# Performance work log

Hardware: AMD Instinct MI355X
Metric: run time of the kernel (lower is better)

## Reference

```python
import jax, jax.numpy as jnp
import numpy as np

N1 = 512
N2 = 512
N = N1 + N2
NEG_SLOPE = 0.2


def _build_edges(n1, n2):
    # inside: fully connected within each set, both directions
    s1, d1 = np.triu_indices(n1, 1)
    s2, d2 = np.triu_indices(n2, 1)
    is_ = np.concatenate([s1, s2 + n1])
    id_ = np.concatenate([d1, d2 + n1])
    inside = np.stack([np.concatenate([is_, id_]), np.concatenate([id_, is_])])
    # cross: fully connected bipartite, both directions
    cs = np.repeat(np.arange(n1), n2)
    cd = np.tile(np.arange(n1, n1 + n2), n1)
    cross = np.stack([np.concatenate([cs, cd]), np.concatenate([cd, cs])])
    # PyG GATConv default add_self_loops=True
    loops = np.arange(n1 + n2)
    self_e = np.stack([loops, loops])
    inside = np.concatenate([inside, self_e], axis=1)
    cross = np.concatenate([cross, self_e], axis=1)
    return inside.astype(np.int32), cross.astype(np.int32)


def setup_inputs() -> dict:
    key = jax.random.key(0)
    ks = jax.random.split(key, 12)
    inside_edge, cross_edge = _build_edges(N1, N2)
    s = 0.1
    return {
        'desc1': jax.random.normal(ks[0], (N1, 128), jnp.float32),
        'desc2': jax.random.normal(ks[1], (N2, 128), jnp.float32),
        'W1': jax.random.normal(ks[2], (128, 128), jnp.float32) * s,
        'a_src1': jax.random.normal(ks[3], (128, 1), jnp.float32) * s,
        'a_dst1': jax.random.normal(ks[4], (128, 1), jnp.float32) * s,
        'b1': jnp.zeros((128,), jnp.float32),
        'W2': jax.random.normal(ks[5], (128, 128), jnp.float32) * s,
        'a_src2': jax.random.normal(ks[6], (1, 128), jnp.float32) * s,
        'a_dst2': jax.random.normal(ks[7], (1, 128), jnp.float32) * s,
        'b2': jnp.zeros((128,), jnp.float32),
        'inside_edge': jnp.asarray(inside_edge),
        'cross_edge': jnp.asarray(cross_edge),
    }


def gat_conv(x, edge_index, W, a_src, a_dst, bias, heads, out_ch, concat):
    # x: [N, F_in]; edge_index: [2, E] (self-loops already included)
    n = x.shape[0]
    src, dst = edge_index[0], edge_index[1]
    h = (x @ W).reshape(n, heads, out_ch)                 # [N, H, C]
    a_s = jnp.sum(h * a_src, axis=-1)                     # [N, H]
    a_d = jnp.sum(h * a_dst, axis=-1)                     # [N, H]
    e = jax.nn.leaky_relu(a_s[src] + a_d[dst], NEG_SLOPE)  # [E, H]
    # segment (scatter) softmax over incoming edges of each dst node
    m = jax.ops.segment_max(e, dst, num_segments=n)
    ex = jnp.exp(e - m[dst])
    denom = jax.ops.segment_sum(ex, dst, num_segments=n)
    alpha = ex / (denom[dst] + 1e-16)                     # [E, H]
    out = jax.ops.segment_sum(alpha[:, :, None] * h[src], dst, num_segments=n)  # [N, H, C]
    out = out.reshape(n, heads * out_ch) if concat else out.mean(axis=1)
    return out + bias


def reference(desc1, desc2, W1, a_src1, a_dst1, b1, W2, a_src2, a_dst2, b2, inside_edge, cross_edge):
    x = jnp.concatenate([desc1, desc2], axis=0)  # [N, 128]
    for _ in range(2):
        x = jax.nn.elu(gat_conv(x, inside_edge, W1, a_src1, a_dst1, b1, 128, 1, True))
        x = jax.nn.elu(gat_conv(x, cross_edge, W1, a_src1, a_dst1, b1, 128, 1, True))
    x = gat_conv(x, cross_edge, W2, a_src2, a_dst2, b2, 1, 128, False)  # [N, 128]
    return x
```

## Files before the change

### kernel.cpp

```cpp
#include <hip/hip_runtime.h>
#include <hip/hip_bf16.h>


typedef __hip_bfloat16 bf16;

__device__ __forceinline__ float b2f(bf16 x) { return __bfloat162float(x); }

__device__ __forceinline__ int detect_bf16(const void* desc1) {
  const unsigned* u = (const unsigned*)desc1;
  int hits = 0;
#pragma unroll 8
  for (int i = 0; i < 256; ++i) {
    unsigned e = (u[i] >> 7) & 0xFFu;
    hits += (e >= 100u && e <= 140u) ? 1 : 0;
  }
  return hits >= 200 ? 1 : 0;
}

__device__ __forceinline__ float load_in(const void* p, int i, int bf) {
  return bf ? b2f(((const bf16*)p)[i]) : ((const float*)p)[i];
}

__global__ __launch_bounds__(256) void prep_kernel(
    const void* __restrict__ desc1, const void* __restrict__ desc2,
    const void* __restrict__ W1,   const void* __restrict__ as1,
    const void* __restrict__ ad1,  const void* __restrict__ b1,
    const void* __restrict__ W2,   const void* __restrict__ as2,
    const void* __restrict__ ad2,  const void* __restrict__ b2,
    float* __restrict__ xt, float* __restrict__ W1f, float* __restrict__ W2f,
    float* __restrict__ vecs, int* __restrict__ flag) {
  const int bf = detect_bf16(desc1);
  if (blockIdx.x == 0 && threadIdx.x == 0) *flag = bf;
  const int total = 131072 + 16384 + 16384 + 6 * 128;
  for (int idx = blockIdx.x * blockDim.x + threadIdx.x; idx < total;
       idx += gridDim.x * blockDim.x) {
    if (idx < 131072) {
      int n = idx & 1023, c = idx >> 10;
      float v = (n < 512) ? load_in(desc1, n * 128 + c, bf)
                          : load_in(desc2, (n - 512) * 128 + c, bf);
      xt[idx] = v;
    } else if (idx < 147456) {
      W1f[idx - 131072] = load_in(W1, idx - 131072, bf);
    } else if (idx < 163840) {
      W2f[idx - 147456] = load_in(W2, idx - 147456, bf);
    } else {
      int i = idx - 163840, o = i & 127;
      float v;
      if      (i < 128) v = load_in(as1, o, bf);
      else if (i < 256) v = load_in(ad1, o, bf);
      else if (i < 384) v = load_in(b1, o, bf);
      else if (i < 512) v = load_in(as2, o, bf);
      else if (i < 640) v = load_in(ad2, o, bf);
      else              v = load_in(b2, o, bf);
      vecs[i] = v;
    }
  }
}

template <int CROSS>
__global__ __launch_bounds__(512, 2) void layer_kernel(
    const float* __restrict__ xt_in, float* __restrict__ xt_out,
    const float* __restrict__ Wf, const float* __restrict__ vecs) {
  __shared__ float    sS[512];
  __shared__ float    sH[512];
  __shared__ unsigned hA[512];
  __shared__ unsigned ISb[512];
  __shared__ unsigned binNext[512];
  __shared__ float2   PRE[512];
  __shared__ float2   SUF[512];
  __shared__ float    red[16];
  __shared__ unsigned wTot[8];
  __shared__ float2   preTot[8];
  __shared__ float2   sufTot[8];

  const int tid  = threadIdx.x;
  const int lane = tid & 63;
  const int wave = tid >> 6;
  const int hd   = blockIdx.x & 127;
  const int S    = blockIdx.x >> 7;
  const int D    = CROSS ? (1 - S) : S;
  const float a_src = vecs[hd], a_dst = vecs[128 + hd], bias = vecs[256 + hd];

  float accS0 = 0.f, accS1 = 0.f, accD0 = 0.f, accD1 = 0.f;
  {
    const float* baseS = xt_in + S * 512 + tid;
    const float* baseD = xt_in + D * 512 + tid;
    for (int kk = 0; kk < 128; kk += 16) {
      float xs[16], xd[16];
#pragma unroll
      for (int u = 0; u < 16; ++u) {
        xs[u] = baseS[(kk + u) * 1024];
        if (CROSS) xd[u] = baseD[(kk + u) * 1024];
      }
#pragma unroll
      for (int u = 0; u < 16; u += 2) {
        float w0 = Wf[(kk + u) * 128 + hd];
        float w1 = Wf[(kk + u + 1) * 128 + hd];
        accS0 = fmaf(xs[u],     w0, accS0);
        accS1 = fmaf(xs[u + 1], w1, accS1);
        if (CROSS) {
          accD0 = fmaf(xd[u],     w0, accD0);
          accD1 = fmaf(xd[u + 1], w1, accD1);
        }
      }
    }
  }
  const float h_src = accS0 + accS1;
  const float h_dst = CROSS ? (accD0 + accD1) : h_src;
  const float s_own = h_src * a_src;
  const float d_own = h_dst * a_dst;

  {
    float mnw = s_own, mxw = s_own;
#pragma unroll
    for (int off = 32; off > 0; off >>= 1) {
      mnw = fminf(mnw, __shfl_down(mnw, off));
      mxw = fmaxf(mxw, __shfl_down(mxw, off));
    }
    if (lane == 0) { red[wave] = mnw; red[8 + wave] = mxw; }
  }
  hA[tid] = 0;
  binNext[tid] = 0;
  __syncthreads();
  const float mn = fminf(fminf(fminf(red[0], red[1]), fminf(red[2], red[3])),
                         fminf(fminf(red[4], red[5]), fminf(red[6], red[7])));
  const float mx = fmaxf(fmaxf(fmaxf(red[8], red[9]), fmaxf(red[10], red[11])),
                         fmaxf(fmaxf(red[12], red[13]), fmaxf(red[14], red[15])));
  const float scale = 512.0f / fmaxf(mx - mn, 1e-20f);

  const int myBin = (int)fminf(fmaxf((s_own - mn) * scale, 0.0f), 511.0f);
  atomicAdd(&hA[myBin], 1u);
  __syncthreads();

  {
    unsigned v = hA[tid];
#pragma unroll
    for (int off = 1; off < 64; off <<= 1) {
      unsigned u = __shfl_up(v, off);
      if (lane >= off) v += u;
    }
    if (lane == 63) wTot[wave] = v;
    __syncthreads();
    unsigned pre = 0;
#pragma unroll
    for (int w = 0; w < 8; ++w) pre += (w < wave) ? wTot[w] : 0u;
    ISb[tid] = v + pre;
    __syncthreads();
  }

  {
    unsigned base = myBin ? ISb[myBin - 1] : 0u;
    unsigned pos = base + atomicAdd(&binNext[myBin], 1u);
    sS[pos] = s_own;
    sH[pos] = h_src;
  }
  __syncthreads();

  {
    const float sv = sS[tid];
    const float hv = sH[tid];
    const float e1 = __expf(sv), e2 = __expf(0.2f * sv);
    float p0 = e2, p1 = e2 * hv;
    float q0 = e1, q1 = e1 * hv;
#pragma unroll
    for (int off = 1; off < 64; off <<= 1) {
      float u0 = __shfl_up(p0, off), u1 = __shfl_up(p1, off);
      if (lane >= off) { p0 += u0; p1 += u1; }
      float v0 = __shfl_down(q0, off), v1 = __shfl_down(q1, off);
      if (lane + off < 64) { q0 += v0; q1 += v1; }
    }
    if (lane == 63) preTot[wave] = make_float2(p0, p1);
    if (lane == 0)  sufTot[wave] = make_float2(q0, q1);
    __syncthreads();
    float a0 = 0.f, a1 = 0.f, b0 = 0.f, b1 = 0.f;
#pragma unroll
    for (int w = 0; w < 8; ++w) {
      float2 pt = preTot[w], st = sufTot[w];
      if (w < wave) { a0 += pt.x; a1 += pt.y; }
      if (w > wave) { b0 += st.x; b1 += st.y; }
    }
    PRE[tid] = make_float2(p0 + a0, p1 + a1);
    SUF[tid] = make_float2(q0 + b0, q1 + b1);
    __syncthreads();
  }

  {
    const float theta = -d_own;
    int b = (int)fminf(fmaxf((theta - mn) * scale, 0.0f), 511.0f);
    unsigned k0 = b ? ISb[b - 1] : 0u;
    unsigned k1 = ISb[b];
    float F1 = __expf(d_own), F2 = __expf(0.2f * d_own);
    float P2 = 0.f, P2h = 0.f, S1 = 0.f, S1h = 0.f;
    if (k0 > 0)   { float2 t2 = PRE[k0 - 1]; P2 = t2.x; P2h = t2.y; }
    if (k1 < 512) { float2 t2 = SUF[k1];     S1 = t2.x; S1h = t2.y; }
    float den = F1 * S1 + F2 * P2;
    float num = F1 * S1h + F2 * P2h;
    for (unsigned e = k0; e < k1; ++e) {
      float se = sS[e], he = sH[e];
      float p = (se >= theta) ? F1 * __expf(se) : F2 * __expf(0.2f * se);
      den += p;
      num = fmaf(p, he, num);
    }
    if (CROSS) {
      float t = h_dst * a_src + d_own;
      float p = __expf(fmaxf(t, 0.2f * t));
      den += p;
      num = fmaf(p, h_dst, num);
    }
    float o = num / (den + 1e-16f) + bias;
    o = (o > 0.f) ? o : expm1f(o);
    xt_out[hd * 1024 + D * 512 + tid] = o;
  }
}

__global__ __launch_bounds__(256, 2) void mm2_kernel(
    const float* __restrict__ xt_in, const float* __restrict__ W2f,
    const float* __restrict__ vecs, float* __restrict__ h2,
    float* __restrict__ s2, float* __restrict__ d2) {
  __shared__ float rs[256], rd[256];
  const int tid = threadIdx.x;
  const int row = blockIdx.x * 2 + (tid >> 7);
  const int c = tid & 127;
  float acc0 = 0.f, acc1 = 0.f;
  for (int kk = 0; kk < 128; kk += 16) {
    float xb[16];
#pragma unroll
    for (int u = 0; u < 16; ++u) xb[u] = xt_in[(kk + u) * 1024 + row];
#pragma unroll
    for (int u = 0; u < 16; u += 2) {
      acc0 = fmaf(xb[u],     W2f[(kk + u) * 128 + c],     acc0);
      acc1 = fmaf(xb[u + 1], W2f[(kk + u + 1) * 128 + c], acc1);
    }
  }
  float acc = acc0 + acc1;
  h2[row * 128 + c] = acc;
  rs[tid] = acc * vecs[384 + c];
  rd[tid] = acc * vecs[512 + c];
  __syncthreads();
  for (int off = 64; off > 0; off >>= 1) {
    if ((tid & 127) < off) { rs[tid] += rs[tid + off]; rd[tid] += rd[tid + off]; }
    __syncthreads();
  }
  if ((tid & 127) == 0) {
    s2[row] = rs[tid];
    d2[row] = rd[tid];
  }
}

__global__ __launch_bounds__(256, 1) void att2_kernel(
    const float* __restrict__ h2, const float* __restrict__ s2,
    const float* __restrict__ d2, const float* __restrict__ vecs,
    void* __restrict__ out, const int* __restrict__ flag) {
  __shared__ __align__(16) float pT[512 * 4];
  const int tid = threadIdx.x;
  const int dstBase = blockIdx.x * 4;
  const int srcBase = (dstBase < 512) ? 512 : 0;

  for (int e = tid; e < 2048; e += 256) {
    int j = e >> 2, ld = e & 3;
    float t = s2[srcBase + j] + d2[dstBase + ld];
    pT[e] = __expf(fmaxf(t, 0.2f * t));
  }
  __syncthreads();

  const int c = tid & 127;
  const int g = tid >> 7;
  const int i0 = dstBase + 2 * g, i1 = i0 + 1;
  float den0 = 0.f, num0 = 0.f, den1 = 0.f, num1 = 0.f;
  const float* hrow = h2 + srcBase * 128 + c;
  for (int j0 = 0; j0 < 512; j0 += 8) {
    float hb[8];
#pragma unroll
    for (int u = 0; u < 8; ++u) hb[u] = hrow[(j0 + u) * 128];
#pragma unroll
    for (int u = 0; u < 8; ++u) {
      float2 pv = *(const float2*)(pT + (j0 + u) * 4 + 2 * g);
      den0 += pv.x; num0 = fmaf(pv.x, hb[u], num0);
      den1 += pv.y; num1 = fmaf(pv.y, hb[u], num1);
    }
  }
  float ts0 = s2[i0] + d2[i0];
  float ps0 = __expf(fmaxf(ts0, 0.2f * ts0));
  den0 += ps0; num0 = fmaf(ps0, h2[i0 * 128 + c], num0);
  float ts1 = s2[i1] + d2[i1];
  float ps1 = __expf(fmaxf(ts1, 0.2f * ts1));
  den1 += ps1; num1 = fmaf(ps1, h2[i1 * 128 + c], num1);

  float o0 = num0 / (den0 + 1e-16f) + vecs[640 + c];
  float o1 = num1 / (den1 + 1e-16f) + vecs[640 + c];
  if (*flag) {
    ((bf16*)out)[i0 * 128 + c] = __float2bfloat16(o0);
    ((bf16*)out)[i1 * 128 + c] = __float2bfloat16(o1);
  } else {
    ((float*)out)[i0 * 128 + c] = o0;
    ((float*)out)[i1 * 128 + c] = o1;
  }
}

extern "C" void kernel_launch(void* const* d_in, const int* in_sizes, int n_in,
                              void* d_out, int out_size, void* d_ws, size_t ws_size,
                              hipStream_t stream) {
  (void)in_sizes; (void)n_in; (void)out_size; (void)ws_size;
  float* ws   = (float*)d_ws;
  float* xtA  = ws;
  float* xtB  = ws + 131072;
  float* h2   = ws + 262144;
  float* W1f  = ws + 393216;
  float* W2f  = ws + 409600;
  float* vecs = ws + 425984;
  float* s2   = ws + 426752;
  float* d2   = ws + 427776;
  int*   flag = (int*)(ws + 428800);

  prep_kernel<<<64, 256, 0, stream>>>(d_in[0], d_in[1], d_in[2], d_in[3],
                                      d_in[4], d_in[5], d_in[6], d_in[7],
                                      d_in[8], d_in[9], xtA, W1f, W2f, vecs, flag);
  layer_kernel<0><<<256, 512, 0, stream>>>(xtA, xtB, W1f, vecs);
  layer_kernel<1><<<256, 512, 0, stream>>>(xtB, xtA, W1f, vecs);
  layer_kernel<0><<<256, 512, 0, stream>>>(xtA, xtB, W1f, vecs);
  layer_kernel<1><<<256, 512, 0, stream>>>(xtB, xtA, W1f, vecs);
  mm2_kernel<<<512, 256, 0, stream>>>(xtA, W2f, vecs, h2, s2, d2);
  att2_kernel<<<256, 256, 0, stream>>>(h2, s2, d2, vecs, d_out, flag);
}
```

Baseline: 180.0 us.

## Fold input conversion prep kernel into first layer and consumers

Removes the separate prep kernel that converted inputs and weights to fp32 and transposed the descriptors. The first layer now reads the raw row-major descriptors directly with vector loads, and every kernel detects the dtype itself. Weight columns are staged in shared memory instead of being read from a converted global copy. This drops one launch and a full transpose pass, but the first layer reads with a 256/512-byte per-thread stride, which may coalesce poorly, and each block repeats the dtype detection.

```diff
diff --git a/kernel.cpp b/kernel.cpp
--- a/kernel.cpp
+++ b/kernel.cpp
@@ -21,46 +21,20 @@
   return bf ? b2f(((const bf16*)p)[i]) : ((const float*)p)[i];
 }
 
-__global__ __launch_bounds__(256) void prep_kernel(
-    const void* __restrict__ desc1, const void* __restrict__ desc2,
-    const void* __restrict__ W1,   const void* __restrict__ as1,
-    const void* __restrict__ ad1,  const void* __restrict__ b1,
-    const void* __restrict__ W2,   const void* __restrict__ as2,
-    const void* __restrict__ ad2,  const void* __restrict__ b2,
-    float* __restrict__ xt, float* __restrict__ W1f, float* __restrict__ W2f,
-    float* __restrict__ vecs, int* __restrict__ flag) {
-  const int bf = detect_bf16(desc1);
-  if (blockIdx.x == 0 && threadIdx.x == 0) *flag = bf;
-  const int total = 131072 + 16384 + 16384 + 6 * 128;
-  for (int idx = blockIdx.x * blockDim.x + threadIdx.x; idx < total;
-       idx += gridDim.x * blockDim.x) {
-    if (idx < 131072) {
-      int n = idx & 1023, c = idx >> 10;
-      float v = (n < 512) ? load_in(desc1, n * 128 + c, bf)
-                          : load_in(desc2, (n - 512) * 128 + c, bf);
-      xt[idx] = v;
-    } else if (idx < 147456) {
-      W1f[idx - 131072] = load_in(W1, idx - 131072, bf);
-    } else if (idx < 163840) {
-      W2f[idx - 147456] = load_in(W2, idx - 147456, bf);
-    } else {
-      int i = idx - 163840, o = i & 127;
-      float v;
-      if      (i < 128) v = load_in(as1, o, bf);
-      else if (i < 256) v = load_in(ad1, o, bf);
-      else if (i < 384) v = load_in(b1, o, bf);
-      else if (i < 512) v = load_in(as2, o, bf);
-      else if (i < 640) v = load_in(ad2, o, bf);
-      else              v = load_in(b2, o, bf);
-      vecs[i] = v;
-    }
-  }
-}
-
-template <int CROSS>
+__device__ __forceinline__ float bflo(unsigned u) {
+  return __uint_as_float(u << 16);
+}
+__device__ __forceinline__ float bfhi(unsigned u) {
+  return __uint_as_float(u & 0xffff0000u);
+}
+
+template <int CROSS, int RAW>
 __global__ __launch_bounds__(512, 2) void layer_kernel(
+    const void* __restrict__ rawx1, const void* __restrict__ rawx2,
     const float* __restrict__ xt_in, float* __restrict__ xt_out,
-    const float* __restrict__ Wf, const float* __restrict__ vecs) {
+    const void* __restrict__ Wraw, const void* __restrict__ asr,
+    const void* __restrict__ adr,  const void* __restrict__ brw) {
+  __shared__ float    wcol[128];
   __shared__ float    sS[512];
   __shared__ float    sH[512];
   __shared__ unsigned hA[512];
@@ -79,10 +53,57 @@
   const int hd   = blockIdx.x & 127;
   const int S    = blockIdx.x >> 7;
   const int D    = CROSS ? (1 - S) : S;
-  const float a_src = vecs[hd], a_dst = vecs[128 + hd], bias = vecs[256 + hd];
-
-  float accS0 = 0.f, accS1 = 0.f, accD0 = 0.f, accD1 = 0.f;
-  {
+  const int bf   = detect_bf16(rawx1);
+
+  if (tid < 128) wcol[tid] = load_in(Wraw, tid * 128 + hd, bf);
+  const float a_src = load_in(asr, hd, bf);
+  const float a_dst = load_in(adr, hd, bf);
+  const float bias  = load_in(brw, hd, bf);
+  __syncthreads();
+
+  float h_src, h_dst;
+  if (RAW) {
+    float acc0 = 0.f, acc1 = 0.f;
+    const char* rowb = (const char*)((S == 0) ? rawx1 : rawx2);
+    if (bf) {
+      const uint4* rp = (const uint4*)(rowb + (size_t)tid * 256);
+      for (int g = 0; g < 2; ++g) {
+        uint4 q[8];
+#pragma unroll
+        for (int u = 0; u < 8; ++u) q[u] = rp[g * 8 + u];
+#pragma unroll
+        for (int u = 0; u < 8; ++u) {
+          const int ch = (g * 8 + u) * 8;
+          acc0 = fmaf(bflo(q[u].x), wcol[ch + 0], acc0);
+          acc1 = fmaf(bfhi(q[u].x), wcol[ch + 1], acc1);
+          acc0 = fmaf(bflo(q[u].y), wcol[ch + 2], acc0);
+          acc1 = fmaf(bfhi(q[u].y), wcol[ch + 3], acc1);
+          acc0 = fmaf(bflo(q[u].z), wcol[ch + 4], acc0);
+          acc1 = fmaf(bfhi(q[u].z), wcol[ch + 5], acc1);
+          acc0 = fmaf(bflo(q[u].w), wcol[ch + 6], acc0);
+          acc1 = fmaf(bfhi(q[u].w), wcol[ch + 7], acc1);
+        }
+      }
+    } else {
+      const float4* rp = (const float4*)(rowb + (size_t)tid * 512);
+      for (int g = 0; g < 4; ++g) {
+        float4 q[8];
+#pragma unroll
+        for (int u = 0; u < 8; ++u) q[u] = rp[g * 8 + u];
+#pragma unroll
+        for (int u = 0; u < 8; ++u) {
+          const int ch = (g * 8 + u) * 4;
+          acc0 = fmaf(q[u].x, wcol[ch + 0], acc0);
+          acc1 = fmaf(q[u].y, wcol[ch + 1], acc1);
+          acc0 = fmaf(q[u].z, wcol[ch + 2], acc0);
+          acc1 = fmaf(q[u].w, wcol[ch + 3], acc1);
+        }
+      }
+    }
+    h_src = acc0 + acc1;
+    h_dst = h_src;
+  } else {
+    float accS0 = 0.f, accS1 = 0.f, accD0 = 0.f, accD1 = 0.f;
     const float* baseS = xt_in + S * 512 + tid;
     const float* baseD = xt_in + D * 512 + tid;
     for (int kk = 0; kk < 128; kk += 16) {
@@ -94,8 +115,8 @@
       }
 #pragma unroll
       for (int u = 0; u < 16; u += 2) {
-        float w0 = Wf[(kk + u) * 128 + hd];
-        float w1 = Wf[(kk + u + 1) * 128 + hd];
+        float w0 = wcol[kk + u];
+        float w1 = wcol[kk + u + 1];
         accS0 = fmaf(xs[u],     w0, accS0);
         accS1 = fmaf(xs[u + 1], w1, accS1);
         if (CROSS) {
@@ -104,9 +125,9 @@
         }
       }
     }
-  }
-  const float h_src = accS0 + accS1;
-  const float h_dst = CROSS ? (accD0 + accD1) : h_src;
+    h_src = accS0 + accS1;
+    h_dst = CROSS ? (accD0 + accD1) : h_src;
+  }
   const float s_own = h_src * a_src;
   const float d_own = h_dst * a_dst;
 
@@ -214,28 +235,47 @@
 }
 
 __global__ __launch_bounds__(256, 2) void mm2_kernel(
-    const float* __restrict__ xt_in, const float* __restrict__ W2f,
-    const float* __restrict__ vecs, float* __restrict__ h2,
-    float* __restrict__ s2, float* __restrict__ d2) {
+    const void* __restrict__ rawd1, const float* __restrict__ xt_in,
+    const void* __restrict__ W2raw, const void* __restrict__ as2r,
+    const void* __restrict__ ad2r,
+    float* __restrict__ h2, float* __restrict__ s2, float* __restrict__ d2v) {
   __shared__ float rs[256], rd[256];
+  const int bf = detect_bf16(rawd1);
   const int tid = threadIdx.x;
   const int row = blockIdx.x * 2 + (tid >> 7);
   const int c = tid & 127;
   float acc0 = 0.f, acc1 = 0.f;
-  for (int kk = 0; kk < 128; kk += 16) {
-    float xb[16];
-#pragma unroll
-    for (int u = 0; u < 16; ++u) xb[u] = xt_in[(kk + u) * 1024 + row];
-#pragma unroll
-    for (int u = 0; u < 16; u += 2) {
-      acc0 = fmaf(xb[u],     W2f[(kk + u) * 128 + c],     acc0);
-      acc1 = fmaf(xb[u + 1], W2f[(kk + u + 1) * 128 + c], acc1);
+  if (bf) {
+    const unsigned short* W2u = (const unsigned short*)W2raw;
+    for (int kk = 0; kk < 128; kk += 16) {
+      float xb[16];
+#pragma unroll
+      for (int u = 0; u < 16; ++u) xb[u] = xt_in[(kk + u) * 1024 + row];
+#pragma unroll
+      for (int u = 0; u < 16; u += 2) {
+        float w0 = __uint_as_float(((unsigned)W2u[(kk + u) * 128 + c]) << 16);
+        float w1 = __uint_as_float(((unsigned)W2u[(kk + u + 1) * 128 + c]) << 16);
+        acc0 = fmaf(xb[u],     w0, acc0);
+        acc1 = fmaf(xb[u + 1], w1, acc1);
+      }
+    }
+  } else {
+    const float* W2f = (const float*)W2raw;
+    for (int kk = 0; kk < 128; kk += 16) {
+      float xb[16];
+#pragma unroll
+      for (int u = 0; u < 16; ++u) xb[u] = xt_in[(kk + u) * 1024 + row];
+#pragma unroll
+      for (int u = 0; u < 16; u += 2) {
+        acc0 = fmaf(xb[u],     W2f[(kk + u) * 128 + c],     acc0);
+        acc1 = fmaf(xb[u + 1], W2f[(kk + u + 1) * 128 + c], acc1);
+      }
     }
   }
   float acc = acc0 + acc1;
   h2[row * 128 + c] = acc;
-  rs[tid] = acc * vecs[384 + c];
-  rd[tid] = acc * vecs[512 + c];
+  rs[tid] = acc * load_in(as2r, c, bf);
+  rd[tid] = acc * load_in(ad2r, c, bf);
   __syncthreads();
   for (int off = 64; off > 0; off >>= 1) {
     if ((tid & 127) < off) { rs[tid] += rs[tid + off]; rd[tid] += rd[tid + off]; }
@@ -243,22 +283,23 @@
   }
   if ((tid & 127) == 0) {
     s2[row] = rs[tid];
-    d2[row] = rd[tid];
+    d2v[row] = rd[tid];
   }
 }
 
 __global__ __launch_bounds__(256, 1) void att2_kernel(
-    const float* __restrict__ h2, const float* __restrict__ s2,
-    const float* __restrict__ d2, const float* __restrict__ vecs,
-    void* __restrict__ out, const int* __restrict__ flag) {
+    const void* __restrict__ rawd1, const float* __restrict__ h2,
+    const float* __restrict__ s2, const float* __restrict__ d2v,
+    const void* __restrict__ b2r, void* __restrict__ out) {
   __shared__ __align__(16) float pT[512 * 4];
+  const int bf = detect_bf16(rawd1);
   const int tid = threadIdx.x;
   const int dstBase = blockIdx.x * 4;
   const int srcBase = (dstBase < 512) ? 512 : 0;
 
   for (int e = tid; e < 2048; e += 256) {
     int j = e >> 2, ld = e & 3;
-    float t = s2[srcBase + j] + d2[dstBase + ld];
+    float t = s2[srcBase + j] + d2v[dstBase + ld];
     pT[e] = __expf(fmaxf(t, 0.2f * t));
   }
   __syncthreads();
@@ -279,16 +320,17 @@
       den1 += pv.y; num1 = fmaf(pv.y, hb[u], num1);
     }
   }
-  float ts0 = s2[i0] + d2[i0];
+  float ts0 = s2[i0] + d2v[i0];
   float ps0 = __expf(fmaxf(ts0, 0.2f * ts0));
   den0 += ps0; num0 = fmaf(ps0, h2[i0 * 128 + c], num0);
-  float ts1 = s2[i1] + d2[i1];
+  float ts1 = s2[i1] + d2v[i1];
   float ps1 = __expf(fmaxf(ts1, 0.2f * ts1));
   den1 += ps1; num1 = fmaf(ps1, h2[i1 * 128 + c], num1);
 
-  float o0 = num0 / (den0 + 1e-16f) + vecs[640 + c];
-  float o1 = num1 / (den1 + 1e-16f) + vecs[640 + c];
-  if (*flag) {
+  float b2c = load_in(b2r, c, bf);
+  float o0 = num0 / (den0 + 1e-16f) + b2c;
+  float o1 = num1 / (den1 + 1e-16f) + b2c;
+  if (bf) {
     ((bf16*)out)[i0 * 128 + c] = __float2bfloat16(o0);
     ((bf16*)out)[i1 * 128 + c] = __float2bfloat16(o1);
   } else {
@@ -301,24 +343,32 @@
                               void* d_out, int out_size, void* d_ws, size_t ws_size,
                               hipStream_t stream) {
   (void)in_sizes; (void)n_in; (void)out_size; (void)ws_size;
-  float* ws   = (float*)d_ws;
-  float* xtA  = ws;
-  float* xtB  = ws + 131072;
-  float* h2   = ws + 262144;
-  float* W1f  = ws + 393216;
-  float* W2f  = ws + 409600;
-  float* vecs = ws + 425984;
-  float* s2   = ws + 426752;
-  float* d2   = ws + 427776;
-  int*   flag = (int*)(ws + 428800);
-
-  prep_kernel<<<64, 256, 0, stream>>>(d_in[0], d_in[1], d_in[2], d_in[3],
-                                      d_in[4], d_in[5], d_in[6], d_in[7],
-                                      d_in[8], d_in[9], xtA, W1f, W2f, vecs, flag);
-  layer_kernel<0><<<256, 512, 0, stream>>>(xtA, xtB, W1f, vecs);
-  layer_kernel<1><<<256, 512, 0, stream>>>(xtB, xtA, W1f, vecs);
-  layer_kernel<0><<<256, 512, 0, stream>>>(xtA, xtB, W1f, vecs);
-  layer_kernel<1><<<256, 512, 0, stream>>>(xtB, xtA, W1f, vecs);
-  mm2_kernel<<<512, 256, 0, stream>>>(xtA, W2f, vecs, h2, s2, d2);
-  att2_kernel<<<256, 256, 0, stream>>>(h2, s2, d2, vecs, d_out, flag);
-}
+  float* ws  = (float*)d_ws;
+  float* xtA = ws;
+  float* xtB = ws + 131072;
+  float* h2  = ws + 262144;
+  float* s2  = ws + 393216;
+  float* d2v = ws + 394240;
+
+  const void* desc1 = d_in[0];
+  const void* desc2 = d_in[1];
+  const void* W1    = d_in[2];
+  const void* as1   = d_in[3];
+  const void* ad1   = d_in[4];
+  const void* b1    = d_in[5];
+  const void* W2    = d_in[6];
+  const void* as2   = d_in[7];
+  const void* ad2   = d_in[8];
+  const void* b2    = d_in[9];
+
+  layer_kernel<0, 1><<<256, 512, 0, stream>>>(desc1, desc2, xtA, xtB,
+                                              W1, as1, ad1, b1);
+  layer_kernel<1, 0><<<256, 512, 0, stream>>>(desc1, desc2, xtB, xtA,
+                                              W1, as1, ad1, b1);
+  layer_kernel<0, 0><<<256, 512, 0, stream>>>(desc1, desc2, xtA, xtB,
+                                              W1, as1, ad1, b1);
+  layer_kernel<1, 0><<<256, 512, 0, stream>>>(desc1, desc2, xtB, xtA,
+                                              W1, as1, ad1, b1);
+  mm2_kernel<<<512, 256, 0, stream>>>(desc1, xtA, W2, as2, ad2, h2, s2, d2v);
+  att2_kernel<<<256, 256, 0, stream>>>(desc1, h2, s2, d2v, b2, d_out);
+}
```

Measured after the change: 222.9 us. 1.24x slower.

## Interleave activation layout in groups of four channels for float4 loads

Applied to the files above, without the earlier changes.

Changes the transposed activation buffer from [channel][node] to [channel/4][node][4], so each thread fetches four channels with one 16-byte load in the attention and second-layer matmul kernels. The producer kernels (prep and the attention output write) are updated to match. This cuts the number of load instructions in the per-head projection loop. In exchange, the per-head output stores become strided by 16 bytes, which lowers write coalescing.

```diff
diff --git a/kernel.cpp b/kernel.cpp
--- a/kernel.cpp
+++ b/kernel.cpp
@@ -38,7 +38,7 @@
       int n = idx & 1023, c = idx >> 10;
       float v = (n < 512) ? load_in(desc1, n * 128 + c, bf)
                           : load_in(desc2, (n - 512) * 128 + c, bf);
-      xt[idx] = v;
+      xt[((c >> 2) * 1024 + n) * 4 + (c & 3)] = v;
     } else if (idx < 147456) {
       W1f[idx - 131072] = load_in(W1, idx - 131072, bf);
     } else if (idx < 163840) {
@@ -83,24 +83,32 @@
 
   float accS0 = 0.f, accS1 = 0.f, accD0 = 0.f, accD1 = 0.f;
   {
-    const float* baseS = xt_in + S * 512 + tid;
-    const float* baseD = xt_in + D * 512 + tid;
-    for (int kk = 0; kk < 128; kk += 16) {
-      float xs[16], xd[16];
-#pragma unroll
-      for (int u = 0; u < 16; ++u) {
-        xs[u] = baseS[(kk + u) * 1024];
-        if (CROSS) xd[u] = baseD[(kk + u) * 1024];
+    const float4* x4 = (const float4*)xt_in;
+    const int nS = S * 512 + tid;
+    const int nD = D * 512 + tid;
+    for (int cc = 0; cc < 32; cc += 8) {
+      float4 xs[8], xd[8];
+#pragma unroll
+      for (int u = 0; u < 8; ++u) {
+        xs[u] = x4[(cc + u) * 1024 + nS];
+        if (CROSS) xd[u] = x4[(cc + u) * 1024 + nD];
       }
 #pragma unroll
-      for (int u = 0; u < 16; u += 2) {
-        float w0 = Wf[(kk + u) * 128 + hd];
-        float w1 = Wf[(kk + u + 1) * 128 + hd];
-        accS0 = fmaf(xs[u],     w0, accS0);
-        accS1 = fmaf(xs[u + 1], w1, accS1);
+      for (int u = 0; u < 8; ++u) {
+        const int k = (cc + u) * 4;
+        const float w0 = Wf[k * 128 + hd];
+        const float w1 = Wf[(k + 1) * 128 + hd];
+        const float w2 = Wf[(k + 2) * 128 + hd];
+        const float w3 = Wf[(k + 3) * 128 + hd];
+        accS0 = fmaf(xs[u].x, w0, accS0);
+        accS1 = fmaf(xs[u].y, w1, accS1);
+        accS0 = fmaf(xs[u].z, w2, accS0);
+        accS1 = fmaf(xs[u].w, w3, accS1);
         if (CROSS) {
-          accD0 = fmaf(xd[u],     w0, accD0);
-          accD1 = fmaf(xd[u + 1], w1, accD1);
+          accD0 = fmaf(xd[u].x, w0, accD0);
+          accD1 = fmaf(xd[u].y, w1, accD1);
+          accD0 = fmaf(xd[u].z, w2, accD0);
+          accD1 = fmaf(xd[u].w, w3, accD1);
         }
       }
     }
@@ -209,7 +217,7 @@
     }
     float o = num / (den + 1e-16f) + bias;
     o = (o > 0.f) ? o : expm1f(o);
-    xt_out[hd * 1024 + D * 512 + tid] = o;
+    xt_out[(((hd >> 2) * 1024) + D * 512 + tid) * 4 + (hd & 3)] = o;
   }
 }
 
@@ -222,14 +230,20 @@
   const int row = blockIdx.x * 2 + (tid >> 7);
   const int c = tid & 127;
   float acc0 = 0.f, acc1 = 0.f;
-  for (int kk = 0; kk < 128; kk += 16) {
-    float xb[16];
-#pragma unroll
-    for (int u = 0; u < 16; ++u) xb[u] = xt_in[(kk + u) * 1024 + row];
-#pragma unroll
-    for (int u = 0; u < 16; u += 2) {
-      acc0 = fmaf(xb[u],     W2f[(kk + u) * 128 + c],     acc0);
-      acc1 = fmaf(xb[u + 1], W2f[(kk + u + 1) * 128 + c], acc1);
+  {
+    const float4* x4 = (const float4*)xt_in;
+    for (int cc = 0; cc < 32; cc += 8) {
+      float4 xb[8];
+#pragma unroll
+      for (int u = 0; u < 8; ++u) xb[u] = x4[(cc + u) * 1024 + row];
+#pragma unroll
+      for (int u = 0; u < 8; ++u) {
+        const int k = (cc + u) * 4;
+        acc0 = fmaf(xb[u].x, W2f[k * 128 + c],       acc0);
+        acc1 = fmaf(xb[u].y, W2f[(k + 1) * 128 + c], acc1);
+        acc0 = fmaf(xb[u].z, W2f[(k + 2) * 128 + c], acc0);
+        acc1 = fmaf(xb[u].w, W2f[(k + 3) * 128 + c], acc1);
+      }
     }
   }
   float acc = acc0 + acc1;
```

Result: faster. 168.9 us (-6.2%).
